# Optimization experiments

Measured on AMD Instinct MI355X. Metric: run time of the kernel, lower is better.

The kernel has to match this reference:

```python
import jax, jax.numpy as jnp
import numpy as np

N, H, B = 500000, 256, 512  # nodes, hidden_dim, number of graphs


def setup_inputs() -> dict:
    key = jax.random.key(0)
    k1, k2, k3, k4 = jax.random.split(key, 4)
    x = jax.random.normal(k1, (N, H), dtype=jnp.float32)
    batch = jnp.sort(jax.random.randint(k2, (N,), 0, B)).astype(jnp.int64)
    # attention_pool params (Linear(H,H) -> Tanh -> Linear(H,1))
    s1 = 1.0 / np.sqrt(H)
    W1 = jax.random.uniform(k3, (H, H), jnp.float32, -s1, s1)
    b1 = jnp.zeros((H,), jnp.float32)
    W2 = jax.random.uniform(k4, (H, 1), jnp.float32, -s1, s1)
    b2 = jnp.zeros((1,), jnp.float32)
    return {"x": x, "batch": batch, "W1": W1, "b1": b1, "W2": W2, "b2": b2}


def reference(x, batch, W1, b1, W2, b2):
    # attention scores per node: Linear -> tanh -> Linear -> scalar
    s = (jnp.tanh(x @ W1 + b1) @ W2 + b2)[:, 0]            # [N]
    # segment-wise softmax over nodes of each graph (numerically stable)
    seg_max = jax.ops.segment_max(s, batch, num_segments=B)  # [B]
    e = jnp.exp(s - seg_max[batch])                          # [N]
    denom = jax.ops.segment_sum(e, batch, num_segments=B)    # [B]
    w = e / denom[batch]                                     # [N]
    attn_pool = jax.ops.segment_sum(x * w[:, None], batch, num_segments=B)  # [B,H]
    # mean pool
    sums = jax.ops.segment_sum(x, batch, num_segments=B)     # [B,H]
    counts = jax.ops.segment_sum(jnp.ones((x.shape[0],), x.dtype), batch, num_segments=B)
    mean_pool = sums / jnp.maximum(counts, 1.0)[:, None]
    # max pool (guard empty segments -> 0, matching zero-init buffer behavior)
    max_pool = jax.ops.segment_max(x, batch, num_segments=B)
    max_pool = jnp.where(counts[:, None] > 0, max_pool, 0.0)
    return jnp.concatenate([mean_pool, max_pool, attn_pool], axis=1)  # [B, 3H]
```

## Files before the change

kernel.cpp:

```cpp
#include <hip/hip_runtime.h>

#define HDIM 256
#define MTILE 64
#define NITER 4
#define APITCH 264
#define PROWS 256
#define CHUNK 16

typedef __attribute__((ext_vector_type(8))) short short8;
typedef __attribute__((ext_vector_type(4))) short short4v;
typedef __attribute__((ext_vector_type(4))) float floatx4;

__device__ __forceinline__ unsigned short f2bf(float f){
  unsigned u = __float_as_uint(f);
  u += 0x7FFFu + ((u>>16)&1u);
  return (unsigned short)(u>>16);
}
__device__ __forceinline__ unsigned fkey(float f){
  unsigned u = __float_as_uint(f);
  return u ^ ((unsigned)((int)u>>31) | 0x80000000u);
}
__device__ __forceinline__ float fdec(unsigned u){
  unsigned b = (u & 0x80000000u) ? (u & 0x7FFFFFFFu) : ~u;
  return __uint_as_float(b);
}

__global__ void k_zero(float* __restrict__ p, int n){
  int i = blockIdx.x*256 + threadIdx.x;
  if (i < n) p[i] = 0.f;
}

__global__ void k_prep(const float* __restrict__ w1, unsigned short* __restrict__ w1t){
  int col = blockIdx.x, k = threadIdx.x;
  w1t[col*HDIM + k] = f2bf(w1[k*HDIM + col]);
}

__global__ void k_bounds(const int* __restrict__ batch, int* __restrict__ segstart,
                         int n, int B){
  int i = blockIdx.x*256 + threadIdx.x;
  if (i >= n) return;
  int b = batch[i];
  int prev = (i == 0) ? -1 : batch[i-1];
  if (prev != b) for (int q = prev+1; q <= b; ++q) segstart[q] = i;
  if (i == n-1) for (int q = b+1; q <= B; ++q) segstart[q] = n;
}

__launch_bounds__(256)
__global__ void k_scores(const float* __restrict__ x,
                         const unsigned short* __restrict__ w1t,
                         const float* __restrict__ b1,
                         const float* __restrict__ w2,
                         const float* __restrict__ b2,
                         float* __restrict__ s, int n)
{
  __shared__ unsigned short As[MTILE*APITCH];
  __shared__ float sp[4][MTILE];
  const int t = threadIdx.x;
  const int wv = t>>6;
  const int lane = t&63;
  const int l15 = lane&15;
  const int quad = lane>>4;
  const long long base = (long long)blockIdx.x * (MTILE*NITER);

  short8 bf[8][4];
  float b1v[4], w2v[4];
  const int cb = wv*64;
  #pragma unroll
  for (int ct=0; ct<4; ++ct){
    int col = cb + ct*16 + l15;
    b1v[ct] = b1[col];
    w2v[ct] = w2[col];
    #pragma unroll
    for (int kc=0; kc<8; ++kc)
      bf[kc][ct] = *(const short8*)(w1t + (size_t)col*HDIM + kc*32 + quad*8);
  }

  const float4* x4 = (const float4*)x;
  for (int it = 0; it < NITER; ++it){
    const long long node0 = base + (long long)it*MTILE;
    if (node0 >= n) break;

    #pragma unroll
    for (int j=0; j<MTILE/4; ++j){
      int f = j*256 + t;
      int row = f>>6, c4 = f&63;
      long long gr = node0 + row;
      float4 v = make_float4(0.f,0.f,0.f,0.f);
      if (gr < n) v = x4[gr*(HDIM/4) + c4];
      short4v p;
      p.x=(short)f2bf(v.x); p.y=(short)f2bf(v.y); p.z=(short)f2bf(v.z); p.w=(short)f2bf(v.w);
      *(short4v*)(As + row*APITCH + c4*4) = p;
    }
    __syncthreads();

    #pragma unroll 1
    for (int rt=0; rt<MTILE/16; ++rt){
      floatx4 acc[4];
      #pragma unroll
      for (int ct=0;ct<4;++ct) acc[ct] = (floatx4){0.f,0.f,0.f,0.f};
      #pragma unroll
      for (int kc=0; kc<8; ++kc){
        short8 a = *(const short8*)(As + (rt*16 + l15)*APITCH + kc*32 + quad*8);
        #pragma unroll
        for (int ct=0; ct<4; ++ct)
          acc[ct] = __builtin_amdgcn_mfma_f32_16x16x32_bf16(a, bf[kc][ct], acc[ct], 0, 0, 0);
      }
      float part[4] = {0.f,0.f,0.f,0.f};
      #pragma unroll
      for (int ct=0; ct<4; ++ct){
        #pragma unroll
        for (int r=0; r<4; ++r){
          float h = acc[ct][r] + b1v[ct];
          float z = fminf(fmaxf(2.f*h, -30.f), 30.f);
          float e = __expf(z);
          part[r] += __fdividef(e-1.f, e+1.f) * w2v[ct];
        }
      }
      #pragma unroll
      for (int off=8; off>=1; off>>=1){
        #pragma unroll
        for (int r=0;r<4;++r) part[r] += __shfl_xor(part[r], off, 64);
      }
      if (l15==0){
        #pragma unroll
        for (int r=0;r<4;++r) sp[wv][rt*16 + quad*4 + r] = part[r];
      }
    }
    __syncthreads();
    if (t < MTILE){
      long long gr = node0 + t;
      if (gr < n) s[gr] = sp[0][t]+sp[1][t]+sp[2][t]+sp[3][t] + b2[0];
    }
  }
}

__global__ void k_seg(float* __restrict__ s, const int* __restrict__ segstart,
                      float* __restrict__ denom, float* __restrict__ counts){
  __shared__ float red[4];
  const int b = blockIdx.x;
  const int t = threadIdx.x;
  const int lane = t&63, wv = t>>6;
  const int start = segstart[b], end = segstart[b+1];

  float m = -INFINITY;
  for (int i = start + t; i < end; i += 256) m = fmaxf(m, s[i]);
  #pragma unroll
  for (int off=32; off>=1; off>>=1) m = fmaxf(m, __shfl_xor(m, off, 64));
  if (lane==0) red[wv] = m;
  __syncthreads();
  m = fmaxf(fmaxf(red[0],red[1]), fmaxf(red[2],red[3]));

  float acc = 0.f;
  for (int i = start + t; i < end; i += 256){
    float e = __expf(s[i] - m);
    s[i] = e; acc += e;
  }
  #pragma unroll
  for (int off=32; off>=1; off>>=1) acc += __shfl_xor(acc, off, 64);
  __syncthreads();
  if (lane==0) red[wv] = acc;
  __syncthreads();
  if (t==0){
    float total = red[0]+red[1]+red[2]+red[3];
    denom[b] = (total > 0.f) ? total : 1.f;
    counts[b] = (float)(end - start);
  }
}

__launch_bounds__(256)
__global__ void k_pool(const float* __restrict__ x, const int* __restrict__ batch,
                       const float* __restrict__ e, const float* __restrict__ denom,
                       float* __restrict__ sums, unsigned* __restrict__ maxu,
                       float* __restrict__ attn, int n){
  const int t = threadIdx.x;
  long long r0 = (long long)blockIdx.x * PROWS;
  if (r0 >= n) return;
  long long r1 = r0 + PROWS; if (r1 > n) r1 = n;
  int curb = batch[r0];
  float rd = 1.f/denom[curb];
  float sum=0.f, att=0.f, mx=-INFINITY;
  long long i = r0;
  while (i < r1){
    if (i + CHUNK <= r1 && batch[i + CHUNK - 1] == curb){
      float v[CHUNK], w[CHUNK];
      #pragma unroll
      for (int k=0;k<CHUNK;++k) v[k] = x[(i+k)*HDIM + t];
      #pragma unroll
      for (int k=0;k<CHUNK;++k) w[k] = e[i+k];
      #pragma unroll
      for (int k=0;k<CHUNK;++k){
        sum += v[k];
        att += v[k]*(w[k]*rd);
        mx = fmaxf(mx, v[k]);
      }
      i += CHUNK;
    } else {
      int b = batch[i];
      if (b != curb){
        atomicAdd(&sums[(size_t)curb*HDIM + t], sum);
        atomicAdd(&attn[(size_t)curb*HDIM + t], att);
        atomicMax(&maxu[(size_t)curb*HDIM + t], fkey(mx));
        curb=b; rd = 1.f/denom[b]; sum=0.f; att=0.f; mx=-INFINITY;
      }
      float v = x[i*HDIM + t];
      sum += v; att += v*(e[i]*rd); mx = fmaxf(mx, v);
      ++i;
    }
  }
  atomicAdd(&sums[(size_t)curb*HDIM + t], sum);
  atomicAdd(&attn[(size_t)curb*HDIM + t], att);
  atomicMax(&maxu[(size_t)curb*HDIM + t], fkey(mx));
}

__global__ void k_fin(const float* __restrict__ sums, const unsigned* __restrict__ maxu,
                      const float* __restrict__ attn, const float* __restrict__ counts,
                      float* __restrict__ out, int bcount){
  int idx = blockIdx.x*256 + threadIdx.x;
  int total = bcount*3*HDIM;
  if (idx >= total) return;
  int b = idx / (3*HDIM);
  int c = idx - b*(3*HDIM);
  float cnt = counts[b];
  float v;
  if (c < HDIM)        v = sums[(size_t)b*HDIM + c] / fmaxf(cnt, 1.f);
  else if (c < 2*HDIM) v = (cnt > 0.f) ? fdec(maxu[(size_t)b*HDIM + (c-HDIM)]) : 0.f;
  else                 v = attn[(size_t)b*HDIM + (c-2*HDIM)];
  out[idx] = v;
}

extern "C" void kernel_launch(void* const* d_in, const int* in_sizes, int n_in,
                              void* d_out, int out_size, void* d_ws, size_t ws_size,
                              hipStream_t stream){
  const float* x   = (const float*)d_in[0];
  const int* batch = (const int*)d_in[1];
  const float* W1  = (const float*)d_in[2];
  const float* b1  = (const float*)d_in[3];
  const float* W2  = (const float*)d_in[4];
  const float* b2  = (const float*)d_in[5];
  float* out = (float*)d_out;
  const int n = in_sizes[1];
  const int B = out_size / (3*HDIM);

  char* w = (char*)d_ws;
  unsigned short* W1T = (unsigned short*)w;
  size_t off = (size_t)HDIM*HDIM*2;
  float* s = (float*)(w + off);
  off += (size_t)((n+3)&~3)*4;
  int* segstart = (int*)(w + off);
  off += (size_t)((B+4)&~3)*4;
  float* stats = (float*)(w + off);
  float* denom  = stats;
  float* counts = stats + B;
  float* sums   = stats + 2*B;
  unsigned* maxu = (unsigned*)(stats + 2*B + (size_t)B*HDIM);
  float* attn   = stats + 2*B + 2*(size_t)B*HDIM;
  int zerowords = 3*B*HDIM;

  hipLaunchKernelGGL(k_zero, dim3((zerowords+255)/256), dim3(256), 0, stream, sums, zerowords);
  hipLaunchKernelGGL(k_prep, dim3(HDIM), dim3(HDIM), 0, stream, W1, W1T);
  hipLaunchKernelGGL(k_bounds, dim3((n+255)/256), dim3(256), 0, stream, batch, segstart, n, B);
  hipLaunchKernelGGL(k_scores, dim3((n + MTILE*NITER - 1)/(MTILE*NITER)), dim3(256), 0, stream,
                     x, W1T, b1, W2, b2, s, n);
  hipLaunchKernelGGL(k_seg, dim3(B), dim3(256), 0, stream, s, segstart, denom, counts);
  hipLaunchKernelGGL(k_pool, dim3((n+PROWS-1)/PROWS), dim3(256), 0, stream,
                     x, batch, s, denom, sums, maxu, attn, n);
  hipLaunchKernelGGL(k_fin, dim3((out_size+255)/256), dim3(256), 0, stream,
                     sums, maxu, attn, counts, out, B);
}
```

Before: 899.0 us.

## Fuse attention softmax and pooling into the score kernel, drop max-subtraction

Merges the score GEMM, the segment softmax and all three poolings into one kernel. Each tile of x is pooled right after its scores are computed, so x is read from global memory once instead of twice. The per-segment max subtraction is dropped: raw exp(score) is accumulated with atomics, and attention sums are divided by the denominator in the final kernel. Zeroing, weight transpose and bounds setup are merged into one launch. The tradeoffs are possible exp overflow for large scores and more atomic traffic.

New measurement: 1.076 ms. 19.7% more time.

```diff
diff --git a/kernel.cpp b/kernel.cpp
--- a/kernel.cpp
+++ b/kernel.cpp
@@ -4,8 +4,6 @@
 #define MTILE 64
 #define NITER 4
 #define APITCH 264
-#define PROWS 256
-#define CHUNK 16
 
 typedef __attribute__((ext_vector_type(8))) short short8;
 typedef __attribute__((ext_vector_type(4))) short short4v;
@@ -25,42 +23,52 @@
   return __uint_as_float(b);
 }
 
-__global__ void k_zero(float* __restrict__ p, int n){
-  int i = blockIdx.x*256 + threadIdx.x;
-  if (i < n) p[i] = 0.f;
-}
-
-__global__ void k_prep(const float* __restrict__ w1, unsigned short* __restrict__ w1t){
-  int col = blockIdx.x, k = threadIdx.x;
-  w1t[col*HDIM + k] = f2bf(w1[k*HDIM + col]);
-}
-
-__global__ void k_bounds(const int* __restrict__ batch, int* __restrict__ segstart,
-                         int n, int B){
-  int i = blockIdx.x*256 + threadIdx.x;
-  if (i >= n) return;
-  int b = batch[i];
-  int prev = (i == 0) ? -1 : batch[i-1];
-  if (prev != b) for (int q = prev+1; q <= b; ++q) segstart[q] = i;
-  if (i == n-1) for (int q = b+1; q <= B; ++q) segstart[q] = n;
+__global__ void k_pre(const float* __restrict__ W1, unsigned short* __restrict__ W1T,
+                      const int* __restrict__ batch, int* __restrict__ segstart,
+                      float* __restrict__ zbuf, int zerowords, int n, int B,
+                      int ZB, int PB){
+  const int bid = blockIdx.x, t = threadIdx.x;
+  if (bid < ZB){
+    int i = bid*256 + t;
+    if (i < zerowords) zbuf[i] = 0.f;
+  } else if (bid < ZB + PB){
+    int col = bid - ZB;
+    W1T[col*HDIM + t] = f2bf(W1[t*HDIM + col]);
+  } else {
+    int i = (bid - ZB - PB)*256 + t;
+    if (i >= n) return;
+    int b = batch[i];
+    int prev = (i == 0) ? -1 : batch[i-1];
+    if (prev != b) for (int q = prev+1; q <= b; ++q) segstart[q] = i;
+    if (i == n-1) for (int q = b+1; q <= B; ++q) segstart[q] = n;
+  }
 }
 
 __launch_bounds__(256)
-__global__ void k_scores(const float* __restrict__ x,
-                         const unsigned short* __restrict__ w1t,
-                         const float* __restrict__ b1,
-                         const float* __restrict__ w2,
-                         const float* __restrict__ b2,
-                         float* __restrict__ s, int n)
+__global__ void k_main(const float* __restrict__ x,
+                       const unsigned short* __restrict__ w1t,
+                       const float* __restrict__ b1,
+                       const float* __restrict__ w2,
+                       const float* __restrict__ b2,
+                       const int* __restrict__ batch,
+                       float* __restrict__ denom,
+                       float* __restrict__ sums,
+                       unsigned* __restrict__ maxu,
+                       float* __restrict__ attn,
+                       int n)
 {
   __shared__ unsigned short As[MTILE*APITCH];
   __shared__ float sp[4][MTILE];
+  __shared__ float earr[MTILE];
+  __shared__ int sbat[MTILE*NITER];
   const int t = threadIdx.x;
   const int wv = t>>6;
   const int lane = t&63;
   const int l15 = lane&15;
   const int quad = lane>>4;
   const long long base = (long long)blockIdx.x * (MTILE*NITER);
+
+  { long long gr = base + t; sbat[t] = (gr < n) ? batch[gr] : -1; }
 
   short8 bf[8][4];
   float b1v[4], w2v[4];
@@ -74,6 +82,10 @@
     for (int kc=0; kc<8; ++kc)
       bf[kc][ct] = *(const short8*)(w1t + (size_t)col*HDIM + kc*32 + quad*8);
   }
+  const float b2v = b2[0];
+
+  float psum = 0.f, patt = 0.f, pmx = -INFINITY;
+  int curb = -1;
 
   const float4* x4 = (const float4*)x;
   for (int it = 0; it < NITER; ++it){
@@ -127,104 +139,77 @@
       }
     }
     __syncthreads();
+
     if (t < MTILE){
       long long gr = node0 + t;
-      if (gr < n) s[gr] = sp[0][t]+sp[1][t]+sp[2][t]+sp[3][t] + b2[0];
-    }
-  }
-}
-
-__global__ void k_seg(float* __restrict__ s, const int* __restrict__ segstart,
-                      float* __restrict__ denom, float* __restrict__ counts){
-  __shared__ float red[4];
-  const int b = blockIdx.x;
-  const int t = threadIdx.x;
-  const int lane = t&63, wv = t>>6;
-  const int start = segstart[b], end = segstart[b+1];
-
-  float m = -INFINITY;
-  for (int i = start + t; i < end; i += 256) m = fmaxf(m, s[i]);
-  #pragma unroll
-  for (int off=32; off>=1; off>>=1) m = fmaxf(m, __shfl_xor(m, off, 64));
-  if (lane==0) red[wv] = m;
-  __syncthreads();
-  m = fmaxf(fmaxf(red[0],red[1]), fmaxf(red[2],red[3]));
-
-  float acc = 0.f;
-  for (int i = start + t; i < end; i += 256){
-    float e = __expf(s[i] - m);
-    s[i] = e; acc += e;
-  }
-  #pragma unroll
-  for (int off=32; off>=1; off>>=1) acc += __shfl_xor(acc, off, 64);
-  __syncthreads();
-  if (lane==0) red[wv] = acc;
-  __syncthreads();
-  if (t==0){
-    float total = red[0]+red[1]+red[2]+red[3];
-    denom[b] = (total > 0.f) ? total : 1.f;
-    counts[b] = (float)(end - start);
-  }
-}
-
-__launch_bounds__(256)
-__global__ void k_pool(const float* __restrict__ x, const int* __restrict__ batch,
-                       const float* __restrict__ e, const float* __restrict__ denom,
-                       float* __restrict__ sums, unsigned* __restrict__ maxu,
-                       float* __restrict__ attn, int n){
-  const int t = threadIdx.x;
-  long long r0 = (long long)blockIdx.x * PROWS;
-  if (r0 >= n) return;
-  long long r1 = r0 + PROWS; if (r1 > n) r1 = n;
-  int curb = batch[r0];
-  float rd = 1.f/denom[curb];
-  float sum=0.f, att=0.f, mx=-INFINITY;
-  long long i = r0;
-  while (i < r1){
-    if (i + CHUNK <= r1 && batch[i + CHUNK - 1] == curb){
-      float v[CHUNK], w[CHUNK];
-      #pragma unroll
-      for (int k=0;k<CHUNK;++k) v[k] = x[(i+k)*HDIM + t];
-      #pragma unroll
-      for (int k=0;k<CHUNK;++k) w[k] = e[i+k];
-      #pragma unroll
-      for (int k=0;k<CHUNK;++k){
-        sum += v[k];
-        att += v[k]*(w[k]*rd);
-        mx = fmaxf(mx, v[k]);
-      }
-      i += CHUNK;
+      float e = 0.f; int b = -1;
+      if (gr < n){
+        float sv = sp[0][t]+sp[1][t]+sp[2][t]+sp[3][t] + b2v;
+        e = __expf(sv);
+        b = sbat[it*MTILE + t];
+      }
+      earr[t] = e;
+      int b0 = __shfl(b, 0, 64);
+      if (__all(b == b0)){
+        float tot = e;
+        #pragma unroll
+        for (int off=32; off>=1; off>>=1) tot += __shfl_xor(tot, off, 64);
+        if (lane==0 && b0 >= 0) atomicAdd(&denom[b0], tot);
+      } else if (b >= 0){
+        atomicAdd(&denom[b], e);
+      }
+    }
+    __syncthreads();
+
+    int rend = (int)((n - node0 < (long long)MTILE) ? (n - node0) : (long long)MTILE);
+#define POOLROW(RR)                                                     \
+    {                                                                   \
+      int b = sbat[it*MTILE + (RR)];                                    \
+      if (b != curb){                                                   \
+        if (curb >= 0){                                                 \
+          size_t o = (size_t)curb*HDIM + t;                             \
+          atomicAdd(&sums[o], psum);                                    \
+          atomicAdd(&attn[o], patt);                                    \
+          atomicMax(&maxu[o], fkey(pmx));                               \
+        }                                                               \
+        curb = b; psum = 0.f; patt = 0.f; pmx = -INFINITY;              \
+      }                                                                 \
+      float v = x[(node0 + (RR))*HDIM + t];                             \
+      psum += v;                                                        \
+      patt = fmaf(v, earr[(RR)], patt);                                 \
+      pmx = fmaxf(pmx, v);                                              \
+    }
+    if (rend == MTILE){
+      #pragma unroll 8
+      for (int r=0; r<MTILE; ++r) POOLROW(r)
     } else {
-      int b = batch[i];
-      if (b != curb){
-        atomicAdd(&sums[(size_t)curb*HDIM + t], sum);
-        atomicAdd(&attn[(size_t)curb*HDIM + t], att);
-        atomicMax(&maxu[(size_t)curb*HDIM + t], fkey(mx));
-        curb=b; rd = 1.f/denom[b]; sum=0.f; att=0.f; mx=-INFINITY;
-      }
-      float v = x[i*HDIM + t];
-      sum += v; att += v*(e[i]*rd); mx = fmaxf(mx, v);
-      ++i;
-    }
-  }
-  atomicAdd(&sums[(size_t)curb*HDIM + t], sum);
-  atomicAdd(&attn[(size_t)curb*HDIM + t], att);
-  atomicMax(&maxu[(size_t)curb*HDIM + t], fkey(mx));
+      for (int r=0; r<rend; ++r) POOLROW(r)
+    }
+#undef POOLROW
+  }
+
+  if (curb >= 0){
+    size_t o = (size_t)curb*HDIM + t;
+    atomicAdd(&sums[o], psum);
+    atomicAdd(&attn[o], patt);
+    atomicMax(&maxu[o], fkey(pmx));
+  }
 }
 
 __global__ void k_fin(const float* __restrict__ sums, const unsigned* __restrict__ maxu,
-                      const float* __restrict__ attn, const float* __restrict__ counts,
+                      const float* __restrict__ attn, const float* __restrict__ denom,
+                      const int* __restrict__ segstart,
                       float* __restrict__ out, int bcount){
   int idx = blockIdx.x*256 + threadIdx.x;
   int total = bcount*3*HDIM;
   if (idx >= total) return;
   int b = idx / (3*HDIM);
   int c = idx - b*(3*HDIM);
-  float cnt = counts[b];
+  int cnt = segstart[b+1] - segstart[b];
   float v;
-  if (c < HDIM)        v = sums[(size_t)b*HDIM + c] / fmaxf(cnt, 1.f);
-  else if (c < 2*HDIM) v = (cnt > 0.f) ? fdec(maxu[(size_t)b*HDIM + (c-HDIM)]) : 0.f;
-  else                 v = attn[(size_t)b*HDIM + (c-2*HDIM)];
+  if (c < HDIM)        v = sums[(size_t)b*HDIM + c] / fmaxf((float)cnt, 1.f);
+  else if (c < 2*HDIM) v = (cnt > 0) ? fdec(maxu[(size_t)b*HDIM + (c-HDIM)]) : 0.f;
+  else                 v = attn[(size_t)b*HDIM + (c-2*HDIM)] / fmaxf(denom[b], 1e-30f);
   out[idx] = v;
 }
 
@@ -244,26 +229,22 @@
   char* w = (char*)d_ws;
   unsigned short* W1T = (unsigned short*)w;
   size_t off = (size_t)HDIM*HDIM*2;
-  float* s = (float*)(w + off);
-  off += (size_t)((n+3)&~3)*4;
   int* segstart = (int*)(w + off);
   off += (size_t)((B+4)&~3)*4;
   float* stats = (float*)(w + off);
   float* denom  = stats;
-  float* counts = stats + B;
-  float* sums   = stats + 2*B;
-  unsigned* maxu = (unsigned*)(stats + 2*B + (size_t)B*HDIM);
-  float* attn   = stats + 2*B + 2*(size_t)B*HDIM;
-  int zerowords = 3*B*HDIM;
-
-  hipLaunchKernelGGL(k_zero, dim3((zerowords+255)/256), dim3(256), 0, stream, sums, zerowords);
-  hipLaunchKernelGGL(k_prep, dim3(HDIM), dim3(HDIM), 0, stream, W1, W1T);
-  hipLaunchKernelGGL(k_bounds, dim3((n+255)/256), dim3(256), 0, stream, batch, segstart, n, B);
-  hipLaunchKernelGGL(k_scores, dim3((n + MTILE*NITER - 1)/(MTILE*NITER)), dim3(256), 0, stream,
-                     x, W1T, b1, W2, b2, s, n);
-  hipLaunchKernelGGL(k_seg, dim3(B), dim3(256), 0, stream, s, segstart, denom, counts);
-  hipLaunchKernelGGL(k_pool, dim3((n+PROWS-1)/PROWS), dim3(256), 0, stream,
-                     x, batch, s, denom, sums, maxu, attn, n);
-  hipLaunchKernelGGL(k_fin, dim3((out_size+255)/256), dim3(256), 0, stream,
-                     sums, maxu, attn, counts, out, B);
-}
+  float* sums   = stats + B;
+  unsigned* maxu = (unsigned*)(stats + B + (size_t)B*HDIM);
+  float* attn   = stats + B + 2*(size_t)B*HDIM;
+  int zerowords = B + 3*B*HDIM;
+
+  int ZB  = (zerowords + 255)/256;
+  int PB  = HDIM;
+  int NBB = (n + 255)/256;
+  hipLaunchKernelGGL(k_pre, dim3(ZB + PB + NBB), dim3(256), 0, stream,
+                     W1, W1T, batch, segstart, stats, zerowords, n, B, ZB, PB);
+  hipLaunchKernelGGL(k_main, dim3((n + MTILE*NITER - 1)/(MTILE*NITER)), dim3(256), 0, stream,
+                     x, W1T, b1, W2, b2, batch, denom, sums, maxu, attn, n);
+  hipLaunchKernelGGL(k_fin, dim3((out_size + 255)/256), dim3(256), 0, stream,
+                     sums, maxu, attn, denom, segstart, out, B);
+}
```
